# Kernel optimization log

Hardware: AMD Instinct MI355X
Metric: run time of the kernel (lower is better)

Reference implementation:

```python
import jax, jax.numpy as jnp
import numpy as np

B, T, EMB_D, HEAD = 8, 2048, 1024, 128


def setup_inputs() -> dict:
    key = jax.random.key(0)
    ks = jax.random.split(key, 7)
    s = 1.0 / np.sqrt(EMB_D)
    return {
        "inputs": jax.random.normal(ks[0], (B, T, EMB_D), dtype=jnp.float32),
        "Wk": jax.random.uniform(ks[1], (EMB_D, HEAD), jnp.float32, -s, s),
        "bk": jax.random.uniform(ks[2], (HEAD,), jnp.float32, -s, s),
        "Wq": jax.random.uniform(ks[3], (EMB_D, HEAD), jnp.float32, -s, s),
        "bq": jax.random.uniform(ks[4], (HEAD,), jnp.float32, -s, s),
        "Wv": jax.random.uniform(ks[5], (EMB_D, HEAD), jnp.float32, -s, s),
        "bv": jax.random.uniform(ks[6], (HEAD,), jnp.float32, -s, s),
    }


def reference(inputs, Wk, bk, Wq, bq, Wv, bv):
    # inputs: [B, T, C]
    Bq, Tq, _ = inputs.shape
    k = inputs @ Wk + bk  # [B, T, H]
    q = inputs @ Wq + bq
    v = inputs @ Wv + bv
    scale = HEAD ** -0.5
    weights = jnp.einsum("bth,bsh->bts", q, k) * scale  # [B, T, T]
    causal = jnp.tril(jnp.ones((Tq, Tq), dtype=bool))
    weights = jnp.where(causal, weights, -jnp.inf)
    # NOTE: original code applies softmax over dim=1 (the query axis), faithfully reproduced
    weights = jax.nn.softmax(weights, axis=1)
    return jnp.einsum("bts,bsh->bth", weights, v)  # [B, T, H]
```

## Files before the change

kernel.cpp:

```cpp
#include <hip/hip_runtime.h>
#include <hip/hip_bf16.h>

#define T_SEQ 2048
#define NBATCH 8
#define EMB 1024
#define HD 128

typedef _Float16 f16_t;
typedef _Float16 f16x8 __attribute__((ext_vector_type(8)));
typedef _Float16 f16x4 __attribute__((ext_vector_type(4)));
typedef float f32x4 __attribute__((ext_vector_type(4)));

#define NEG_INF (-__builtin_inff())


__global__ __launch_bounds__(256) void prep_w(
    const float* __restrict__ Wk, const float* __restrict__ bk,
    const float* __restrict__ Wq, const float* __restrict__ bq,
    const float* __restrict__ Wv, const float* __restrict__ bv,
    f16_t* __restrict__ w2, float* __restrict__ biasc) {
    int n = blockIdx.x;
    const float scale = 0.08838834764831845f;
    const float* W; const float* bias; float sc; int col;
    if (n < 128)      { W = Wq; bias = bq; sc = scale; col = n; }
    else if (n < 256) { W = Wk; bias = bk; sc = 1.0f;  col = n - 128; }
    else              { W = Wv; bias = bv; sc = 1.0f;  col = n - 256; }
    int t = threadIdx.x;
    if (t < 128) {
        int k0 = t * 8;
        f16x8 v;
        #pragma unroll
        for (int i = 0; i < 8; ++i) v[i] = (f16_t)(W[(size_t)(k0 + i) * HD + col] * sc);
        *(f16x8*)&w2[(size_t)(n >> 4) * 16384 + (size_t)(k0 >> 3) * 128 + (n & 15) * 8] = v;
    }
    if (t == 0) biasc[n] = bias[col] * sc;
}

__global__ __launch_bounds__(256) void qkv_gemm(
    const float* __restrict__ X, const f16_t* __restrict__ w2,
    const float* __restrict__ biasc,
    f16_t* __restrict__ q2, f16_t* __restrict__ k2, f16_t* __restrict__ v2) {
    __shared__ f16_t Xs[64 * 40];

    int bid = blockIdx.x;
    int r8 = bid & 7, g = bid >> 3;
    int band = (g / 3) * 8 + r8;
    int i = g % 3;
    int m0 = band * 64, n0 = i * 128;
    int tid = threadIdx.x;
    int lane = tid & 63, w = tid >> 6;
    int quad = lane >> 4, l15 = lane & 15;
    int msub = (w & 1) * 32, nsub = (w >> 1) * 64;

    int srow = tid >> 2;
    int scol = (tid & 3) * 8;

    f32x4 acc[2][4] = {};

    for (int kc = 0; kc < EMB; kc += 32) {
        __syncthreads();
        {
            const float* src = X + (size_t)(m0 + srow) * EMB + kc + scol;
            float4 f0 = *(const float4*)src;
            float4 f1 = *(const float4*)(src + 4);
            union { f16_t h[8]; uint4 u; } pk;
            pk.h[0] = (f16_t)f0.x; pk.h[1] = (f16_t)f0.y;
            pk.h[2] = (f16_t)f0.z; pk.h[3] = (f16_t)f0.w;
            pk.h[4] = (f16_t)f1.x; pk.h[5] = (f16_t)f1.y;
            pk.h[6] = (f16_t)f1.z; pk.h[7] = (f16_t)f1.w;
            *(uint4*)&Xs[srow * 40 + scol] = pk.u;
        }
        __syncthreads();

        f16x8 afr[2];
        #pragma unroll
        for (int mf = 0; mf < 2; ++mf)
            afr[mf] = *(const f16x8*)&Xs[(msub + mf * 16 + l15) * 40 + quad * 8];
        #pragma unroll
        for (int nf = 0; nf < 4; ++nf) {
            int ntile = (n0 + nsub + nf * 16) >> 4;
            f16x8 bfr = *(const f16x8*)&w2[(size_t)ntile * 16384 + (size_t)((kc >> 3) + quad) * 128 + l15 * 8];
            #pragma unroll
            for (int mf = 0; mf < 2; ++mf)
                acc[mf][nf] = __builtin_amdgcn_mfma_f32_16x16x32_f16(afr[mf], bfr, acc[mf][nf], 0, 0, 0);
        }
    }

    #pragma unroll
    for (int nf = 0; nf < 4; ++nf) {
        int ng = n0 + nsub + nf * 16 + l15;
        float bval = biasc[ng];
        #pragma unroll
        for (int mf = 0; mf < 2; ++mf) {
            int rowg = m0 + msub + mf * 16 + quad * 4;
            f32x4 a = acc[mf][nf];
            if (ng < 256) {
                f16_t* dst = (ng < 128) ? q2 : k2;
                int c = ng & 127;
                #pragma unroll
                for (int r = 0; r < 4; ++r) {
                    int row = rowg + r;
                    dst[(size_t)(row >> 4) * 2048 + (c >> 3) * 128 + (row & 15) * 8 + (c & 7)]
                        = (f16_t)(a[r] + bval);
                }
            } else {
                int h = ng - 256;
                f16x4 hv;
                #pragma unroll
                for (int r = 0; r < 4; ++r) hv[r] = (f16_t)(a[r] + bval);
                *(f16x4*)&v2[(size_t)(rowg >> 3) * 1024 + h * 8 + (rowg & 7)] = hv;
            }
        }
    }
}

__global__ __launch_bounds__(256, 8) void col_stats(
    const f16_t* __restrict__ q2, const f16_t* __restrict__ k2,
    float* __restrict__ pstats) {
    __shared__ float pl[4][16];
    int bid = blockIdx.x;
    int b = bid & 7;
    int item = bid >> 3;
    int j, slab;
    if (item < 128)      { j = item >> 2;            slab = item & 3; }
    else if (item < 224) { int r = item - 128; j = 32 + r / 3; slab = r % 3; }
    else if (item < 288) { int r = item - 224; j = 64 + (r >> 1); slab = r & 1; }
    else                 { j = 96 + (item - 288);    slab = 0; }

    int sb = j << 4;
    int tid = threadIdx.x, lane = tid & 63, w = tid >> 6;
    int quad = lane >> 4, l15 = lane & 15;
    int brow = b * 128;

    f16x8 bfr[4];
    const f16_t* kt = k2 + (size_t)(brow + j) * 2048 + l15 * 8;
    #pragma unroll
    for (int c = 0; c < 4; ++c) bfr[c] = *(const f16x8*)(kt + (c * 4 + quad) * 128);

    float lacc = 0.f;
    int scol = sb + l15;
    int it_end = 128 - j;
    int ie = min(slab * 32 + 32, it_end);
    for (int it = slab * 32 + w; it < ie; it += 4) {
        int t0 = sb + (it << 4);
        const f16_t* qt = q2 + (size_t)(brow + (t0 >> 4)) * 2048 + l15 * 8;
        f32x4 s = {};
        #pragma unroll
        for (int c = 0; c < 4; ++c) {
            f16x8 afr = *(const f16x8*)(qt + (c * 4 + quad) * 128);
            s = __builtin_amdgcn_mfma_f32_16x16x32_f16(afr, bfr[c], s, 0, 0, 0);
        }
        #pragma unroll
        for (int r = 0; r < 4; ++r) {
            int t = t0 + quad * 4 + r;
            if (t >= scol) lacc += __expf(s[r]);
        }
    }
    lacc += __shfl_xor(lacc, 16, 64);
    lacc += __shfl_xor(lacc, 32, 64);
    if (quad == 0) pl[w][l15] = lacc;
    __syncthreads();
    if (tid < 16) {
        float L = pl[0][tid] + pl[1][tid] + pl[2][tid] + pl[3][tid];
        pstats[(((size_t)b * 128 + j) * 4 + slab) * 16 + tid] = L;
    }
}

__global__ __launch_bounds__(256) void cs_final(
    const float* __restrict__ pstats, float* __restrict__ stats) {
    int idx = blockIdx.x * 256 + threadIdx.x;
    int b = idx >> 11, s = idx & 2047;
    int j = s >> 4, col = s & 15;
    int nslab = (159 - j) >> 5;
    const float* p = pstats + (((size_t)b * 128 + j) * 4) * 16 + col;
    float L = 0.f;
    for (int i = 0; i < nslab; ++i) L += p[(size_t)i * 16];
    stats[(size_t)b * T_SEQ + s] = 1.0f / L;
}

__global__ __launch_bounds__(256, 4) void attn_out(
    const f16_t* __restrict__ q2, const f16_t* __restrict__ k2,
    const f16_t* __restrict__ v2, const float* __restrict__ stats,
    float* __restrict__ out) {
    __shared__ f16_t Pl[4][16 * 40];
    __shared__ float obuf[2048];
    int bid = blockIdx.x;
    int b = bid & 7;
    int j = 127 - (bid >> 3);
    int trow = j << 4;
    int tid = threadIdx.x, lane = tid & 63, w = tid >> 6;
    int quad = lane >> 4, l15 = lane & 15;
    int brow = b * 128;
    size_t base = (size_t)b * T_SEQ;

    f16x8 afr[4];
    {
        const f16_t* qt = q2 + (size_t)(brow + j) * 2048 + l15 * 8;
        #pragma unroll
        for (int c = 0; c < 4; ++c) afr[c] = *(const f16x8*)(qt + (c * 4 + quad) * 128);
    }

    f32x4 o[8] = {};
    f16_t* myP = Pl[w];

    int nch = (j + 2) >> 1;
    for (int c = w; c < nch; c += 4) {
        int sb = c << 5;
        f16x8 vfr[8];
        {
            const f16_t* vb = v2 + ((base + sb) >> 3) * 1024 + quad * 1024 + l15 * 8;
            #pragma unroll
            for (int nf = 0; nf < 8; ++nf) vfr[nf] = *(const f16x8*)(vb + nf * 128);
        }
        #pragma unroll
        for (int sub = 0; sub < 2; ++sub) {
            const f16_t* kt = k2 + (size_t)(brow + (sb >> 4) + sub) * 2048 + l15 * 8;
            f32x4 s = {};
            #pragma unroll
            for (int cc = 0; cc < 4; ++cc) {
                f16x8 bfr = *(const f16x8*)(kt + (cc * 4 + quad) * 128);
                s = __builtin_amdgcn_mfma_f32_16x16x32_f16(afr[cc], bfr, s, 0, 0, 0);
            }
            int scol = sb + sub * 16 + l15;
            float invl = stats[base + scol];
            #pragma unroll
            for (int r = 0; r < 4; ++r) {
                int t = trow + quad * 4 + r;
                float pv = __expf(s[r]) * invl;
                if (scol > t) pv = 0.f;
                myP[(quad * 4 + r) * 40 + sub * 16 + l15] = (f16_t)pv;
            }
        }
        f16x8 pa = *(const f16x8*)&myP[l15 * 40 + quad * 8];
        #pragma unroll
        for (int nf = 0; nf < 8; ++nf)
            o[nf] = __builtin_amdgcn_mfma_f32_16x16x32_f16(pa, vfr[nf], o[nf], 0, 0, 0);
    }

    for (int i2 = tid; i2 < 2048; i2 += 256) obuf[i2] = 0.f;
    __syncthreads();
    #pragma unroll
    for (int nf = 0; nf < 8; ++nf)
        #pragma unroll
        for (int r = 0; r < 4; ++r)
            atomicAdd(&obuf[(quad * 4 + r) * 128 + nf * 16 + l15], o[nf][r]);
    __syncthreads();
    for (int i2 = tid; i2 < 2048; i2 += 256)
        out[(base + trow + (i2 >> 7)) * HD + (i2 & 127)] = obuf[i2];
}

extern "C" void kernel_launch(void* const* d_in, const int* in_sizes, int n_in,
                              void* d_out, int out_size, void* d_ws, size_t ws_size,
                              hipStream_t stream) {
    const float* X  = (const float*)d_in[0];
    const float* Wk = (const float*)d_in[1];
    const float* bk = (const float*)d_in[2];
    const float* Wq = (const float*)d_in[3];
    const float* bq = (const float*)d_in[4];
    const float* Wv = (const float*)d_in[5];
    const float* bv = (const float*)d_in[6];
    float* out = (float*)d_out;

    char* ws = (char*)d_ws;
    const size_t W2_B    = 24 * 16384 * 2;
    const size_t BIAS_B  = 2048;
    const size_t QKV_B   = (size_t)NBATCH * T_SEQ * HD * 2;
    const size_t STAT_B  = (size_t)NBATCH * T_SEQ * 4;
    f16_t* w2     = (f16_t*)ws;
    float* biasc  = (float*)(ws + W2_B);
    f16_t* q2     = (f16_t*)(ws + W2_B + BIAS_B);
    f16_t* k2     = (f16_t*)(ws + W2_B + BIAS_B + QKV_B);
    f16_t* v2     = (f16_t*)(ws + W2_B + BIAS_B + 2 * QKV_B);
    float* stats  = (float*)(ws + W2_B + BIAS_B + 3 * QKV_B);
    float* pstats = (float*)(ws + W2_B + BIAS_B + 3 * QKV_B + STAT_B);

    prep_w<<<dim3(384), dim3(256), 0, stream>>>(Wk, bk, Wq, bq, Wv, bv, w2, biasc);
    qkv_gemm<<<dim3(768), dim3(256), 0, stream>>>(X, w2, biasc, q2, k2, v2);
    col_stats<<<dim3(2560), dim3(256), 0, stream>>>(q2, k2, pstats);
    cs_final<<<dim3(64), dim3(256), 0, stream>>>(pstats, stats);
    attn_out<<<dim3(1024), dim3(256), 0, stream>>>(q2, k2, v2, stats, out);
}
```

Baseline: 210.0 us.

## Retile column-stats and attention kernels with LDS staging and atomic split-K

Column-stats now has each block hold a 64-column K tile in registers and stream 64-row Q tiles through LDS via global_load_lds. Partial column sums are combined with global atomics after a zeroing kernel, replacing the pstats reduction kernel. Attention output now processes 32 query rows per block against 64-key K/V chunks staged in LDS, splits long rows into slabs, and atomically accumulates into a pre-zeroed output. This raises data reuse per load and balances the causal workload, at the cost of extra atomics, more syncthreads, and an added zeroing pass.

Result: faster. 185.1 us (-11.9%).

```diff
diff --git a/kernel.cpp b/kernel.cpp
--- a/kernel.cpp
+++ b/kernel.cpp
@@ -11,8 +11,12 @@
 typedef _Float16 f16x4 __attribute__((ext_vector_type(4)));
 typedef float f32x4 __attribute__((ext_vector_type(4)));
 
-#define NEG_INF (-__builtin_inff())
-
+
+__device__ __forceinline__ void g2l(const f16_t* g, f16_t* l) {
+    __builtin_amdgcn_global_load_lds(
+        (const __attribute__((address_space(1))) unsigned int*)g,
+        (__attribute__((address_space(3))) unsigned int*)l, 16, 0, 0);
+}
 
 __global__ __launch_bounds__(256) void prep_w(
     const float* __restrict__ Wk, const float* __restrict__ bk,
@@ -114,139 +118,179 @@
     }
 }
 
-__global__ __launch_bounds__(256, 8) void col_stats(
+__global__ __launch_bounds__(256) void zero_all(float4* __restrict__ out4,
+                                                float4* __restrict__ colsum4) {
+    int bid = blockIdx.x;
+    if (bid < 2048) out4[(size_t)bid * 256 + threadIdx.x] = make_float4(0.f, 0.f, 0.f, 0.f);
+    else if (bid - 2048 < 16) colsum4[(size_t)(bid - 2048) * 256 + threadIdx.x] = make_float4(0.f, 0.f, 0.f, 0.f);
+}
+
+__global__ __launch_bounds__(256, 4) void col_stats(
     const f16_t* __restrict__ q2, const f16_t* __restrict__ k2,
-    float* __restrict__ pstats) {
-    __shared__ float pl[4][16];
+    float* __restrict__ colsum) {
+    __shared__ __align__(16) f16_t Ql[4 * 2048];
+
     int bid = blockIdx.x;
     int b = bid & 7;
-    int item = bid >> 3;
-    int j, slab;
-    if (item < 128)      { j = item >> 2;            slab = item & 3; }
-    else if (item < 224) { int r = item - 128; j = 32 + r / 3; slab = r % 3; }
-    else if (item < 288) { int r = item - 224; j = 64 + (r >> 1); slab = r & 1; }
-    else                 { j = 96 + (item - 288);    slab = 0; }
-
-    int sb = j << 4;
-    int tid = threadIdx.x, lane = tid & 63, w = tid >> 6;
-    int quad = lane >> 4, l15 = lane & 15;
-    int brow = b * 128;
-
-    f16x8 bfr[4];
-    const f16_t* kt = k2 + (size_t)(brow + j) * 2048 + l15 * 8;
-    #pragma unroll
-    for (int c = 0; c < 4; ++c) bfr[c] = *(const f16x8*)(kt + (c * 4 + quad) * 128);
-
-    float lacc = 0.f;
-    int scol = sb + l15;
-    int it_end = 128 - j;
-    int ie = min(slab * 32 + 32, it_end);
-    for (int it = slab * 32 + w; it < ie; it += 4) {
-        int t0 = sb + (it << 4);
-        const f16_t* qt = q2 + (size_t)(brow + (t0 >> 4)) * 2048 + l15 * 8;
-        f32x4 s = {};
-        #pragma unroll
-        for (int c = 0; c < 4; ++c) {
-            f16x8 afr = *(const f16x8*)(qt + (c * 4 + quad) * 128);
-            s = __builtin_amdgcn_mfma_f32_16x16x32_f16(afr, bfr[c], s, 0, 0, 0);
-        }
-        #pragma unroll
-        for (int r = 0; r < 4; ++r) {
-            int t = t0 + quad * 4 + r;
-            if (t >= scol) lacc += __expf(s[r]);
-        }
-    }
-    lacc += __shfl_xor(lacc, 16, 64);
-    lacc += __shfl_xor(lacc, 32, 64);
-    if (quad == 0) pl[w][l15] = lacc;
-    __syncthreads();
-    if (tid < 16) {
-        float L = pl[0][tid] + pl[1][tid] + pl[2][tid] + pl[3][tid];
-        pstats[(((size_t)b * 128 + j) * 4 + slab) * 16 + tid] = L;
-    }
-}
-
-__global__ __launch_bounds__(256) void cs_final(
-    const float* __restrict__ pstats, float* __restrict__ stats) {
-    int idx = blockIdx.x * 256 + threadIdx.x;
-    int b = idx >> 11, s = idx & 2047;
-    int j = s >> 4, col = s & 15;
-    int nslab = (159 - j) >> 5;
-    const float* p = pstats + (((size_t)b * 128 + j) * 4) * 16 + col;
-    float L = 0.f;
-    for (int i = 0; i < nslab; ++i) L += p[(size_t)i * 16];
-    stats[(size_t)b * T_SEQ + s] = 1.0f / L;
-}
-
-__global__ __launch_bounds__(256, 4) void attn_out(
-    const f16_t* __restrict__ q2, const f16_t* __restrict__ k2,
-    const f16_t* __restrict__ v2, const float* __restrict__ stats,
-    float* __restrict__ out) {
-    __shared__ f16_t Pl[4][16 * 40];
-    __shared__ float obuf[2048];
-    int bid = blockIdx.x;
-    int b = bid & 7;
-    int j = 127 - (bid >> 3);
-    int trow = j << 4;
+    int item = 143 - (bid >> 3);
+    int cg = 0, slab = 0, cum = 0;
+    for (int c = 0; c < 32; ++c) {
+        int n = (32 - c + 3) >> 2;
+        if (item < cum + n) { cg = c; slab = item - cum; break; }
+        cum += n;
+    }
+    int tc0 = cg + slab * 4, tc1 = min(tc0 + 4, 32);
+
     int tid = threadIdx.x, lane = tid & 63, w = tid >> 6;
     int quad = lane >> 4, l15 = lane & 15;
     int brow = b * 128;
     size_t base = (size_t)b * T_SEQ;
 
-    f16x8 afr[4];
-    {
-        const f16_t* qt = q2 + (size_t)(brow + j) * 2048 + l15 * 8;
-        #pragma unroll
-        for (int c = 0; c < 4; ++c) afr[c] = *(const f16x8*)(qt + (c * 4 + quad) * 128);
-    }
-
-    f32x4 o[8] = {};
-    f16_t* myP = Pl[w];
-
-    int nch = (j + 2) >> 1;
-    for (int c = w; c < nch; c += 4) {
-        int sb = c << 5;
-        f16x8 vfr[8];
-        {
-            const f16_t* vb = v2 + ((base + sb) >> 3) * 1024 + quad * 1024 + l15 * 8;
-            #pragma unroll
-            for (int nf = 0; nf < 8; ++nf) vfr[nf] = *(const f16x8*)(vb + nf * 128);
-        }
-        #pragma unroll
-        for (int sub = 0; sub < 2; ++sub) {
-            const f16_t* kt = k2 + (size_t)(brow + (sb >> 4) + sub) * 2048 + l15 * 8;
+    f16x8 bfrs[4][4];
+    #pragma unroll
+    for (int st = 0; st < 4; ++st) {
+        const f16_t* kt = k2 + (size_t)(brow + cg * 4 + st) * 2048 + l15 * 8;
+        #pragma unroll
+        for (int kf = 0; kf < 4; ++kf)
+            bfrs[st][kf] = *(const f16x8*)(kt + (kf * 4 + quad) * 128);
+    }
+
+    float lacc[4] = {0.f, 0.f, 0.f, 0.f};
+
+    for (int tc = tc0; tc < tc1; ++tc) {
+        int tb = tc * 64;
+        __syncthreads();
+        const f16_t* qsrc = q2 + (size_t)(brow + tc * 4) * 2048;
+        #pragma unroll
+        for (int i = 0; i < 4; ++i)
+            g2l(qsrc + i * 2048 + tid * 8, Ql + i * 2048 + tid * 8);
+        __syncthreads();
+
+        f16x8 afr[4];
+        #pragma unroll
+        for (int kf = 0; kf < 4; ++kf)
+            afr[kf] = *(const f16x8*)&Ql[w * 2048 + (kf * 4 + quad) * 128 + l15 * 8];
+        #pragma unroll
+        for (int st = 0; st < 4; ++st) {
             f32x4 s = {};
             #pragma unroll
-            for (int cc = 0; cc < 4; ++cc) {
-                f16x8 bfr = *(const f16x8*)(kt + (cc * 4 + quad) * 128);
-                s = __builtin_amdgcn_mfma_f32_16x16x32_f16(afr[cc], bfr, s, 0, 0, 0);
+            for (int kf = 0; kf < 4; ++kf)
+                s = __builtin_amdgcn_mfma_f32_16x16x32_f16(afr[kf], bfrs[st][kf], s, 0, 0, 0);
+            int scol = cg * 64 + st * 16 + l15;
+            #pragma unroll
+            for (int r = 0; r < 4; ++r) {
+                int t = tb + w * 16 + quad * 4 + r;
+                if (t >= scol) lacc[st] += __expf(s[r]);
             }
-            int scol = sb + sub * 16 + l15;
-            float invl = stats[base + scol];
+        }
+    }
+
+    #pragma unroll
+    for (int st = 0; st < 4; ++st) {
+        float v = lacc[st];
+        v += __shfl_xor(v, 16, 64);
+        v += __shfl_xor(v, 32, 64);
+        if (quad == 0) atomicAdd(&colsum[base + cg * 64 + st * 16 + l15], v);
+    }
+}
+
+__global__ __launch_bounds__(256) void inv_l(
+    const float* __restrict__ colsum, float* __restrict__ invl) {
+    int i = blockIdx.x * 256 + threadIdx.x;
+    invl[i] = 1.0f / colsum[i];
+}
+
+__global__ __launch_bounds__(256, 4) void attn_out(
+    const f16_t* __restrict__ q2, const f16_t* __restrict__ k2,
+    const f16_t* __restrict__ v2, const float* __restrict__ invl,
+    float* __restrict__ out) {
+    __shared__ __align__(16) f16_t Kl[4 * 2048];
+    __shared__ __align__(16) f16_t Vl[8 * 1024];
+    __shared__ __align__(16) f16_t Pl[32 * 72];
+
+    int bid = blockIdx.x;
+    int b = bid & 7;
+    int item = 159 - (bid >> 3);
+    int g = 0, slab = 0, cum = 0;
+    for (int gg = 0; gg < 64; ++gg) {
+        int n = (((gg >> 1) + 1) + 7) >> 3;
+        if (item < cum + n) { g = gg; slab = item - cum; break; }
+        cum += n;
+    }
+    int nch = (g >> 1) + 1;
+    int c0 = slab * 8, c1 = min(c0 + 8, nch);
+    int trow = g * 32;
+
+    int tid = threadIdx.x, lane = tid & 63, w = tid >> 6;
+    int quad = lane >> 4, l15 = lane & 15;
+    int brow = b * 128;
+    size_t base = (size_t)b * T_SEQ;
+
+    f16x8 qfr[2][4];
+    #pragma unroll
+    for (int tt = 0; tt < 2; ++tt) {
+        const f16_t* qt = q2 + (size_t)(brow + 2 * g + tt) * 2048 + l15 * 8;
+        #pragma unroll
+        for (int kf = 0; kf < 4; ++kf)
+            qfr[tt][kf] = *(const f16x8*)(qt + (kf * 4 + quad) * 128);
+    }
+
+    f32x4 o[2][2] = {};
+
+    for (int c = c0; c < c1; ++c) {
+        int sb = c * 64;
+        __syncthreads();
+        const f16_t* ksrc = k2 + (size_t)(brow + (sb >> 4)) * 2048;
+        const f16_t* vsrc = v2 + (((size_t)base + sb) >> 3) * 1024;
+        #pragma unroll
+        for (int i = 0; i < 4; ++i) {
+            g2l(ksrc + i * 2048 + tid * 8, Kl + i * 2048 + tid * 8);
+            g2l(vsrc + i * 2048 + tid * 8, Vl + i * 2048 + tid * 8);
+        }
+        __syncthreads();
+
+        float iv = invl[base + sb + w * 16 + l15];
+        int scol = sb + w * 16 + l15;
+        f16x8 bfr[4];
+        #pragma unroll
+        for (int kf = 0; kf < 4; ++kf)
+            bfr[kf] = *(const f16x8*)&Kl[w * 2048 + (kf * 4 + quad) * 128 + l15 * 8];
+        #pragma unroll
+        for (int tt = 0; tt < 2; ++tt) {
+            f32x4 s = {};
+            #pragma unroll
+            for (int kf = 0; kf < 4; ++kf)
+                s = __builtin_amdgcn_mfma_f32_16x16x32_f16(qfr[tt][kf], bfr[kf], s, 0, 0, 0);
             #pragma unroll
             for (int r = 0; r < 4; ++r) {
-                int t = trow + quad * 4 + r;
-                float pv = __expf(s[r]) * invl;
-                if (scol > t) pv = 0.f;
-                myP[(quad * 4 + r) * 40 + sub * 16 + l15] = (f16_t)pv;
+                int t = trow + tt * 16 + quad * 4 + r;
+                float pv = (t >= scol) ? __expf(s[r]) * iv : 0.f;
+                Pl[(tt * 16 + quad * 4 + r) * 72 + w * 16 + l15] = (f16_t)pv;
             }
         }
-        f16x8 pa = *(const f16x8*)&myP[l15 * 40 + quad * 8];
-        #pragma unroll
-        for (int nf = 0; nf < 8; ++nf)
-            o[nf] = __builtin_amdgcn_mfma_f32_16x16x32_f16(pa, vfr[nf], o[nf], 0, 0, 0);
-    }
-
-    for (int i2 = tid; i2 < 2048; i2 += 256) obuf[i2] = 0.f;
-    __syncthreads();
-    #pragma unroll
-    for (int nf = 0; nf < 8; ++nf)
-        #pragma unroll
-        for (int r = 0; r < 4; ++r)
-            atomicAdd(&obuf[(quad * 4 + r) * 128 + nf * 16 + l15], o[nf][r]);
-    __syncthreads();
-    for (int i2 = tid; i2 < 2048; i2 += 256)
-        out[(base + trow + (i2 >> 7)) * HD + (i2 & 127)] = obuf[i2];
+        __syncthreads();
+
+        #pragma unroll
+        for (int kf2 = 0; kf2 < 2; ++kf2) {
+            f16x8 pa0 = *(const f16x8*)&Pl[(l15) * 72 + kf2 * 32 + quad * 8];
+            f16x8 pa1 = *(const f16x8*)&Pl[(16 + l15) * 72 + kf2 * 32 + quad * 8];
+            #pragma unroll
+            for (int hh = 0; hh < 2; ++hh) {
+                f16x8 vfr = *(const f16x8*)&Vl[(kf2 * 4 + quad) * 1024 + (w * 32 + hh * 16 + l15) * 8];
+                o[0][hh] = __builtin_amdgcn_mfma_f32_16x16x32_f16(pa0, vfr, o[0][hh], 0, 0, 0);
+                o[1][hh] = __builtin_amdgcn_mfma_f32_16x16x32_f16(pa1, vfr, o[1][hh], 0, 0, 0);
+            }
+        }
+    }
+
+    #pragma unroll
+    for (int tt = 0; tt < 2; ++tt)
+        #pragma unroll
+        for (int hh = 0; hh < 2; ++hh)
+            #pragma unroll
+            for (int r = 0; r < 4; ++r)
+                atomicAdd(&out[(base + trow + tt * 16 + quad * 4 + r) * HD + w * 32 + hh * 16 + l15],
+                          o[tt][hh][r]);
 }
 
 extern "C" void kernel_launch(void* const* d_in, const int* in_sizes, int n_in,
@@ -265,18 +309,19 @@
     const size_t W2_B    = 24 * 16384 * 2;
     const size_t BIAS_B  = 2048;
     const size_t QKV_B   = (size_t)NBATCH * T_SEQ * HD * 2;
-    const size_t STAT_B  = (size_t)NBATCH * T_SEQ * 4;
+    const size_t CS_B    = (size_t)NBATCH * T_SEQ * 4;
     f16_t* w2     = (f16_t*)ws;
     float* biasc  = (float*)(ws + W2_B);
     f16_t* q2     = (f16_t*)(ws + W2_B + BIAS_B);
     f16_t* k2     = (f16_t*)(ws + W2_B + BIAS_B + QKV_B);
     f16_t* v2     = (f16_t*)(ws + W2_B + BIAS_B + 2 * QKV_B);
-    float* stats  = (float*)(ws + W2_B + BIAS_B + 3 * QKV_B);
-    float* pstats = (float*)(ws + W2_B + BIAS_B + 3 * QKV_B + STAT_B);
+    float* colsum = (float*)(ws + W2_B + BIAS_B + 3 * QKV_B);
+    float* invl   = (float*)(ws + W2_B + BIAS_B + 3 * QKV_B + CS_B);
 
     prep_w<<<dim3(384), dim3(256), 0, stream>>>(Wk, bk, Wq, bq, Wv, bv, w2, biasc);
     qkv_gemm<<<dim3(768), dim3(256), 0, stream>>>(X, w2, biasc, q2, k2, v2);
-    col_stats<<<dim3(2560), dim3(256), 0, stream>>>(q2, k2, pstats);
-    cs_final<<<dim3(64), dim3(256), 0, stream>>>(pstats, stats);
-    attn_out<<<dim3(1024), dim3(256), 0, stream>>>(q2, k2, v2, stats, out);
-}
+    zero_all<<<dim3(2064), dim3(256), 0, stream>>>((float4*)out, (float4*)colsum);
+    col_stats<<<dim3(1152), dim3(256), 0, stream>>>(q2, k2, colsum);
+    inv_l<<<dim3(64), dim3(256), 0, stream>>>(colsum, invl);
+    attn_out<<<dim3(1280), dim3(256), 0, stream>>>(q2, k2, v2, invl, out);
+}
```
